# Kernel optimization log

Hardware: AMD Instinct MI355X
Metric: run time of the kernel (lower is better)

Reference implementation:

```python
import jax, jax.numpy as jnp
import numpy as np


def setup_inputs() -> dict:
    key = jax.random.key(0)
    k1, k2 = jax.random.split(key)
    B, C, H, W = 8, 64, 128, 512
    image_tensor = jax.random.normal(k1, (B, C, H, W), dtype=jnp.float32)
    # positive metric depths in ~[1, 56] m
    depth = jax.random.uniform(k2, (B, H, W), dtype=jnp.float32) * 55.0 + 1.0
    fx = fy = 500.0; cx = 512.0; cy = 128.0  # intrinsics for original 1024x256 image
    camera_k = jnp.tile(jnp.array([[fx, 0.0, cx], [0.0, fy, cy], [0.0, 0.0, 1.0]],
                                  dtype=jnp.float32)[None], (B, 1, 1))
    meter_per_pixel = jnp.full((1,), 0.25, dtype=jnp.float32)
    return {"image_tensor": image_tensor, "camera_k": camera_k, "depth": depth,
            "meter_per_pixel": meter_per_pixel, "sat_width": 512,
            "ori_grdH": 256, "ori_grdW": 1024}


def reference(image_tensor, camera_k, depth, meter_per_pixel, sat_width, ori_grdH, ori_grdW):
    B, C, H, W = image_tensor.shape
    half = sat_width // 2
    mpp = meter_per_pixel.reshape(())

    # scale intrinsics from original image size to feature-map size (rows 0 and 1)
    row_scale = jnp.array([W / ori_grdW, H / ori_grdH, 1.0], dtype=jnp.float32)
    ck = camera_k * row_scale[None, :, None]
    k_inv = jnp.linalg.inv(ck)  # [B,3,3]

    # back-project pixel grid: xyz_w[b,h,w,:] = K^-1 @ [u,v,1]
    v, u = jnp.meshgrid(jnp.arange(H, dtype=jnp.float32),
                        jnp.arange(W, dtype=jnp.float32), indexing='ij')
    uv1 = jnp.stack([u, v, jnp.ones_like(u)], axis=-1)          # [H,W,3]
    xyz_w = jnp.einsum('bij,hwj->bhwi', k_inv, uv1)             # [B,H,W,3]
    # depth is already at (H,W): bilinear same-size resize is identity
    xyz = (xyz_w * depth[..., None] * 1.2).reshape(B * H * W, 3)

    feats = image_tensor.transpose(0, 2, 3, 1).reshape(B * H * W, C)

    # voxelize x,z (torch .long() truncates toward zero)
    x = jnp.trunc(xyz[:, 0] / mpp).astype(jnp.int32)
    z = jnp.trunc(xyz[:, 2] / mpp).astype(jnp.int32)
    y = xyz[:, 1]
    b = jnp.repeat(jnp.arange(B, dtype=jnp.int32), H * W)

    kept = (x >= -half) & (x <= half - 1) & (z >= -half) & (z <= half - 1)
    max_h = jnp.max(jnp.where(kept, y, -jnp.inf))
    xx = x + half
    zz = z + half
    h = max_h - y  # height key; the last entry per voxel (max h) survives dedup

    # voxel rank (same encoding as torch); out-of-bounds points get a sentinel
    rank0 = zz * (sat_width * B) + (xx + 1) * B + b
    SENT = sat_width * sat_width * B + B
    rank0 = jnp.where(kept, rank0, SENT)

    # torch: sort by h, then stable sort by rank0  == lexsort(primary=rank0, secondary=h)
    order = jnp.lexsort((h, rank0))
    r_s = rank0[order]
    f_s = feats[order]
    b_s, xx_s, zz_s = b[order], xx[order], zz[order]

    # keep the last point of each rank0 group (highest h in that voxel)
    is_last = jnp.concatenate([r_s[:-1] != r_s[1:], jnp.array([True])])
    valid = is_last & (r_s != SENT)

    flat = b_s * (sat_width * sat_width) + xx_s * sat_width + zz_s
    flat = jnp.where(valid, flat, B * sat_width * sat_width)  # invalid -> OOB, dropped

    final = jnp.zeros((B * sat_width * sat_width, C), dtype=jnp.float32)
    final = final.at[flat].set(f_s, mode='drop')
    return final.reshape(B, sat_width, sat_width, C).transpose(0, 3, 1, 2)
```

## Files before the change

kernel.cpp:

```cpp
#include <hip/hip_runtime.h>

#define BB 8
#define CC 64
#define HH 128
#define WW 512
#define SS 512
#define HALF 256
#define HWP (HH * WW)
#define BHW (BB * HWP)
#define CELLS (BB * SS * SS)

__device__ __forceinline__ unsigned int order_f32(float f) {
    unsigned int u = __float_as_uint(f);
    return (u & 0x80000000u) ? ~u : (u | 0x80000000u);
}

__global__ __launch_bounds__(256) void proj_kernel(
    const float* __restrict__ camera_k,
    const float* __restrict__ depth,
    const float* __restrict__ mpp_p,
    unsigned long long* __restrict__ keys)
{
    __shared__ float sk[9];
    const int idx = blockIdx.x * 256 + threadIdx.x;
    const int b = idx >> 16;

    if (threadIdx.x == 0) {
        const float rs[3] = {0.5f, 0.5f, 1.0f};
        double a[9];
        #pragma unroll
        for (int i = 0; i < 3; ++i)
            #pragma unroll
            for (int j = 0; j < 3; ++j)
                a[i*3 + j] = (double)__fmul_rn(camera_k[b*9 + i*3 + j], rs[i]);
        double det = a[0]*(a[4]*a[8]-a[5]*a[7])
                   - a[1]*(a[3]*a[8]-a[5]*a[6])
                   + a[2]*(a[3]*a[7]-a[4]*a[6]);
        double inv[9];
        inv[0] =  (a[4]*a[8]-a[5]*a[7])/det;
        inv[1] = -(a[1]*a[8]-a[2]*a[7])/det;
        inv[2] =  (a[1]*a[5]-a[2]*a[4])/det;
        inv[3] = -(a[3]*a[8]-a[5]*a[6])/det;
        inv[4] =  (a[0]*a[8]-a[2]*a[6])/det;
        inv[5] = -(a[0]*a[5]-a[2]*a[3])/det;
        inv[6] =  (a[3]*a[7]-a[4]*a[6])/det;
        inv[7] = -(a[0]*a[7]-a[1]*a[6])/det;
        inv[8] =  (a[0]*a[4]-a[1]*a[3])/det;
        #pragma unroll
        for (int i = 0; i < 9; ++i) sk[i] = (float)inv[i];
    }
    __syncthreads();

    const int rem = idx & (HWP - 1);
    const int v = rem >> 9;
    const int u = rem & (WW - 1);
    const float d = depth[idx];
    const float mpp = mpp_p[0];
    const float uf = (float)u, vf = (float)v;

    float xw = __fadd_rn(__fadd_rn(__fmul_rn(sk[0], uf), __fmul_rn(sk[1], vf)), sk[2]);
    float yw = __fadd_rn(__fadd_rn(__fmul_rn(sk[3], uf), __fmul_rn(sk[4], vf)), sk[5]);
    float zw = __fadd_rn(__fadd_rn(__fmul_rn(sk[6], uf), __fmul_rn(sk[7], vf)), sk[8]);
    float x3 = __fmul_rn(__fmul_rn(xw, d), 1.2f);
    float y3 = __fmul_rn(__fmul_rn(yw, d), 1.2f);
    float z3 = __fmul_rn(__fmul_rn(zw, d), 1.2f);

    int xi = (int)truncf(__fdiv_rn(x3, mpp));
    int zi = (int)truncf(__fdiv_rn(z3, mpp));

    if (xi >= -HALF && xi <= HALF - 1 && zi >= -HALF && zi <= HALF - 1) {
        int cell = (b << 18) | ((xi + HALF) << 9) | (zi + HALF);
        unsigned long long key =
            ((unsigned long long)order_f32(y3) << 32) | (unsigned int)(~idx);
        atomicMin(&keys[cell], key);
    }
}

__global__ __launch_bounds__(256) void scatter_kernel(
    const float* __restrict__ img,
    const unsigned long long* __restrict__ keys,
    float* __restrict__ out)
{
    const int n   = blockIdx.x;
    const int xcd = n & 7;
    const int s   = n >> 3;
    const int cg  = xcd * 2 + (s & 1);
    const int bq  = s >> 1;

    const int q     = bq * 256 + threadIdx.x;
    const int c0    = cg << 2;
    const int cell0 = q << 2;
    const int b     = cell0 >> 18;
    const int local = cell0 & (SS * SS - 1);

    const ulonglong2* kp = (const ulonglong2*)keys + (size_t)q * 2;
    const ulonglong2 ka = kp[0];
    const ulonglong2 kb = kp[1];
    const unsigned long long k[4] = {ka.x, ka.y, kb.x, kb.y};

    int  rem[4];
    bool has[4];
    #pragma unroll
    for (int i = 0; i < 4; ++i) {
        has[i] = (k[i] != ~0ull);
        rem[i] = (int)((~(unsigned int)(k[i] & 0xFFFFFFFFull)) & (HWP - 1));
    }

    const float* plane0 = img + ((size_t)(b * CC + c0)) * HWP;
    float*       op     = out + ((size_t)(b * CC + c0)) * (size_t)(SS * SS) + local;

    float v[4][4];
    #pragma unroll
    for (int c = 0; c < 4; ++c) {
        const float* pl = plane0 + (size_t)c * HWP;
        #pragma unroll
        for (int i = 0; i < 4; ++i)
            v[c][i] = has[i] ? pl[rem[i]] : 0.0f;
    }
    #pragma unroll
    for (int c = 0; c < 4; ++c) {
        float4 f4 = make_float4(v[c][0], v[c][1], v[c][2], v[c][3]);
        *(float4*)(op + (size_t)c * (SS * SS)) = f4;
    }
}

extern "C" void kernel_launch(void* const* d_in, const int* in_sizes, int n_in,
                              void* d_out, int out_size, void* d_ws, size_t ws_size,
                              hipStream_t stream) {
    const float* img      = (const float*)d_in[0];
    const float* camera_k = (const float*)d_in[1];
    const float* depth    = (const float*)d_in[2];
    const float* mpp      = (const float*)d_in[3];

    unsigned long long* keys = (unsigned long long*)d_ws;

    hipMemsetAsync(keys, 0xFF, (size_t)CELLS * sizeof(unsigned long long), stream);

    proj_kernel<<<BHW / 256, 256, 0, stream>>>(camera_k, depth, mpp, keys);

    scatter_kernel<<<32768, 256, 0, stream>>>(img, keys, (float*)d_out);
}
```

Measured before the change: 765.3 us.

## Transpose image to channel-last so scatter gathers contiguous feature rows

```diff
diff --git a/kernel.cpp b/kernel.cpp
--- a/kernel.cpp
+++ b/kernel.cpp
@@ -76,51 +76,75 @@
     }
 }
 
+__global__ __launch_bounds__(256) void transpose_kernel(
+    const float* __restrict__ img,
+    float* __restrict__ img_t)
+{
+    __shared__ float tile[64][65];
+    const int gp0  = blockIdx.x * 64;
+    const int b    = gp0 >> 16;
+    const int p0   = gp0 & (HWP - 1);
+    const int lane = threadIdx.x & 63;
+    const int grp  = threadIdx.x >> 6;
+
+    const float* src = img + (size_t)b * CC * HWP + p0;
+    #pragma unroll
+    for (int i = 0; i < 16; ++i) {
+        int ch = grp * 16 + i;
+        tile[lane][ch] = src[(size_t)ch * HWP + lane];
+    }
+    __syncthreads();
+    float* dst = img_t + (size_t)gp0 * CC;
+    #pragma unroll
+    for (int i = 0; i < 16; ++i) {
+        int p = grp * 16 + i;
+        dst[(size_t)p * CC + lane] = tile[p][lane];
+    }
+}
+
 __global__ __launch_bounds__(256) void scatter_kernel(
-    const float* __restrict__ img,
+    const float* __restrict__ img_t,
     const unsigned long long* __restrict__ keys,
     float* __restrict__ out)
 {
-    const int n   = blockIdx.x;
-    const int xcd = n & 7;
-    const int s   = n >> 3;
-    const int cg  = xcd * 2 + (s & 1);
-    const int bq  = s >> 1;
+    __shared__ float sT[128 * 64];
+    __shared__ int   sRem[128];
 
-    const int q     = bq * 256 + threadIdx.x;
-    const int c0    = cg << 2;
-    const int cell0 = q << 2;
+    const int cell0 = blockIdx.x * 128;
     const int b     = cell0 >> 18;
+    const int t     = threadIdx.x;
+    const int w     = t >> 6;
+    const int l     = t & 63;
+
+    if (t < 128) {
+        unsigned long long k = keys[cell0 + t];
+        sRem[t] = (k == ~0ull) ? -1
+                : (int)((~(unsigned int)(k & 0xFFFFFFFFull)) & (HWP - 1));
+    }
+    __syncthreads();
+
+    const size_t bHWP = (size_t)b * HWP;
+    #pragma unroll 8
+    for (int i = 0; i < 32; ++i) {
+        int cell = w * 32 + i;
+        int r = sRem[cell];
+        float val = 0.0f;
+        if (r >= 0)
+            val = img_t[((bHWP + (size_t)r) << 6) + l];
+        sT[(cell << 6) + (l ^ (cell & 31))] = val;
+    }
+    __syncthreads();
+
     const int local = cell0 & (SS * SS - 1);
-
-    const ulonglong2* kp = (const ulonglong2*)keys + (size_t)q * 2;
-    const ulonglong2 ka = kp[0];
-    const ulonglong2 kb = kp[1];
-    const unsigned long long k[4] = {ka.x, ka.y, kb.x, kb.y};
-
-    int  rem[4];
-    bool has[4];
+    float* op = out + (size_t)b * CC * (SS * SS) + local;
     #pragma unroll
-    for (int i = 0; i < 4; ++i) {
-        has[i] = (k[i] != ~0ull);
-        rem[i] = (int)((~(unsigned int)(k[i] & 0xFFFFFFFFull)) & (HWP - 1));
-    }
-
-    const float* plane0 = img + ((size_t)(b * CC + c0)) * HWP;
-    float*       op     = out + ((size_t)(b * CC + c0)) * (size_t)(SS * SS) + local;
-
-    float v[4][4];
-    #pragma unroll
-    for (int c = 0; c < 4; ++c) {
-        const float* pl = plane0 + (size_t)c * HWP;
-        #pragma unroll
-        for (int i = 0; i < 4; ++i)
-            v[c][i] = has[i] ? pl[rem[i]] : 0.0f;
-    }
-    #pragma unroll
-    for (int c = 0; c < 4; ++c) {
-        float4 f4 = make_float4(v[c][0], v[c][1], v[c][2], v[c][3]);
-        *(float4*)(op + (size_t)c * (SS * SS)) = f4;
+    for (int j = 0; j < 16; ++j) {
+        int c = w * 16 + j;
+        float v0 = sT[((l)      << 6) + (c ^ (l & 31))];
+        float v1 = sT[((l + 64) << 6) + (c ^ (l & 31))];
+        float* oc = op + (size_t)c * (SS * SS);
+        oc[l]      = v0;
+        oc[64 + l] = v1;
     }
 }
 
@@ -133,10 +157,11 @@
     const float* mpp      = (const float*)d_in[3];
 
     unsigned long long* keys = (unsigned long long*)d_ws;
+    float* img_t = (float*)((char*)d_ws + ((size_t)32 << 20));
 
     hipMemsetAsync(keys, 0xFF, (size_t)CELLS * sizeof(unsigned long long), stream);
 
+    transpose_kernel<<<BHW / 64, 256, 0, stream>>>(img, img_t);
     proj_kernel<<<BHW / 256, 256, 0, stream>>>(camera_k, depth, mpp, keys);
-
-    scatter_kernel<<<32768, 256, 0, stream>>>(img, keys, (float*)d_out);
+    scatter_kernel<<<CELLS / 128, 256, 0, stream>>>(img_t, keys, (float*)d_out);
 }
```

New measurement: 844.9 us. 10.4% more time.
